# Kernel optimization log

Hardware: AMD Instinct MI355X
Metric: run time of the kernel (lower is better)

## Reference

```python
import jax, jax.numpy as jnp
import numpy as np

# physical constants (init_kwargs)
M1 = 1.0; M2 = 1.0; M3 = 1.0
L1 = 1.0; L2 = 1.0; L3 = 1.0
G = 9.81


def _kin(td):
    # td: [6] = (theta1, theta2, theta3, dth1, dth2, dth3)
    th, dth = td[:3], td[3:]
    dx1 = dth[0] * L1 * jnp.cos(th[0])
    dy1 = dth[0] * L1 * jnp.sin(th[0])
    dx2 = dx1 + dth[1] * L2 * jnp.cos(th[1])
    dy2 = dy1 + dth[1] * L2 * jnp.sin(th[1])
    dx3 = dx2 + dth[2] * L3 * jnp.cos(th[2])
    dy3 = dy2 + dth[2] * L3 * jnp.sin(th[2])
    vs1 = dx1 * dx1 + dy1 * dy1
    vs2 = dx2 * dx2 + dy2 * dy2
    vs3 = dx3 * dx3 + dy3 * dy3
    return 0.5 * (M1 * vs1 + M2 * vs2 + M3 * vs3)


def _pot(td):
    th = td[:3]
    y1 = -L1 * jnp.cos(th[0])
    y2 = y1 - L2 * jnp.cos(th[1])
    y3 = y2 - L3 * jnp.cos(th[2])
    return (M1 * G * (y1 + L1)
            + M2 * G * (y2 + L1 + L2)
            + M3 * G * (y3 + L1 + L2 + L3))


def _hamiltonian(y):
    # y: [6] = (theta, p_theta). Mass matrix = Hessian of kin w.r.t. velocity slots.
    Mmat = jax.hessian(_kin)(y)[3:6, 3:6]          # 3x3 mass matrix M(theta)
    p = y[3:6]
    dth = p @ jnp.linalg.inv(Mmat)                 # p_theta -> d_theta (M symmetric)
    K = _kin(jnp.concatenate([y[:3], dth]))
    return K + _pot(y)


def _dyn(y):
    g = jax.grad(_hamiltonian)(y)                  # dH/d(theta,p)
    return jnp.concatenate([g[3:6], -g[:3]])       # (dq, dp)


def setup_inputs() -> dict:
    key = jax.random.key(0)
    y = jax.random.normal(key, (2097152, 6), dtype=jnp.float32)
    t = jnp.zeros((1,), dtype=jnp.float32)
    return {"t": t, "y": y}


def reference(t, y):
    # t is unused by the dynamics (autonomous system), kept for API fidelity.
    return jax.vmap(_dyn)(y)
```

## Files before the change

kernel.cpp:

```cpp
#include <hip/hip_runtime.h>


#define GACC 9.81f

typedef float f32x4 __attribute__((ext_vector_type(4)));

__device__ __forceinline__ void dyn6(float th1, float th2, float th3,
                                     float p1, float p2, float p3,
                                     float* __restrict__ o) {
    float s1, c1, s2, c2, s3, c3;
    __sincosf(th1, &s1, &c1);
    __sincosf(th2, &s2, &c2);
    __sincosf(th3, &s3, &c3);
    float c12 = c1 * c2 + s1 * s2, s12 = s1 * c2 - c1 * s2;
    float c13 = c1 * c3 + s1 * s3, s13 = s1 * c3 - c1 * s3;
    float c23 = c2 * c3 + s2 * s3, s23 = s2 * c3 - c2 * s3;
    float A11 = 2.0f - c23 * c23;
    float A12 = c23 * c13 - 2.0f * c12;
    float A13 = 2.0f * (c12 * c23 - c13);
    float A22 = 3.0f - c13 * c13;
    float A23 = 2.0f * c12 * c13 - 3.0f * c23;
    float A33 = 6.0f - 4.0f * c12 * c12;
    float det = 3.0f * A11 + 2.0f * c12 * A12 + c13 * A13;
    float inv = 1.0f / det;
    float dth1 = (A11 * p1 + A12 * p2 + A13 * p3) * inv;
    float dth2 = (A12 * p1 + A22 * p2 + A23 * p3) * inv;
    float dth3 = (A13 * p1 + A23 * p2 + A33 * p3) * inv;
    o[0] = dth1;
    o[1] = dth2;
    o[2] = dth3;
    float t12 = dth1 * dth2 * s12;
    float t13 = dth1 * dth3 * s13;
    float t23 = dth2 * dth3 * s23;
    o[3] = -2.0f * t12 - t13 - 3.0f * GACC * s1;
    o[4] =  2.0f * t12 - t23 - 2.0f * GACC * s2;
    o[5] =  t13 + t23 - GACC * s3;
}

#define WFENCE() __builtin_amdgcn_fence(__ATOMIC_SEQ_CST, "wavefront")

__global__ __launch_bounds__(256, 6) void pend3_kernel(const f32x4* __restrict__ y4,
                                                       f32x4* __restrict__ out4,
                                                       int nTiles) {
    __shared__ f32x4 s[768];
    const int wave = threadIdx.x >> 6;
    const int lane = threadIdx.x & 63;
    f32x4* sw = s + wave * 192;

    for (int tile = blockIdx.x; tile < nTiles; tile += gridDim.x) {
        const size_t gbase = (size_t)tile * 768 + wave * 192;

#pragma unroll
        for (int k = 0; k < 3; ++k)
            sw[lane + 64 * k] = y4[gbase + lane + 64 * k];
        WFENCE();

        const int j0 = 3 * lane;
        f32x4 a = sw[j0];
        f32x4 b = sw[j0 + 1];
        f32x4 c = sw[j0 + 2];

        float o0[6], o1[6];
        dyn6(a.x, a.y, a.z, a.w, b.x, b.y, o0);
        dyn6(b.z, b.w, c.x, c.y, c.z, c.w, o1);

        f32x4 r0 = {o0[0], o0[1], o0[2], o0[3]};
        f32x4 r1 = {o0[4], o0[5], o1[0], o1[1]};
        f32x4 r2 = {o1[2], o1[3], o1[4], o1[5]};
        sw[j0]     = r0;
        sw[j0 + 1] = r1;
        sw[j0 + 2] = r2;
        WFENCE();

#pragma unroll
        for (int k = 0; k < 3; ++k) {
            f32x4 v = sw[lane + 64 * k];
            __builtin_nontemporal_store(v, &out4[gbase + lane + 64 * k]);
        }
        WFENCE();
    }
}

extern "C" void kernel_launch(void* const* d_in, const int* in_sizes, int n_in,
                              void* d_out, int out_size, void* d_ws, size_t ws_size,
                              hipStream_t stream) {
    const f32x4* y4 = (const f32x4*)d_in[1];
    f32x4* out4 = (f32x4*)d_out;
    int nQuads = in_sizes[1] / 4;
    int nTiles = nQuads / 768;
    int grid = nTiles < 2048 ? nTiles : 2048;
    pend3_kernel<<<grid, 256, 0, stream>>>(y4, out4, nTiles);
}
```

Baseline: 20.82 us.

## Process two tiles per block with all loads issued upfront, no grid-stride loop

Replaces the persistent grid-stride loop with a fixed grid where each block handles exactly two 768-quad tiles. Both tiles' global loads are issued up front into registers so the second tile's memory latency overlaps the first tile's compute and stores. It drops the occupancy hint from the launch bounds and assumes the input size is a multiple of 1536 quads, with no tail handling.

```diff
diff --git a/kernel.cpp b/kernel.cpp
--- a/kernel.cpp
+++ b/kernel.cpp
@@ -39,46 +39,61 @@
 
 #define WFENCE() __builtin_amdgcn_fence(__ATOMIC_SEQ_CST, "wavefront")
 
-__global__ __launch_bounds__(256, 6) void pend3_kernel(const f32x4* __restrict__ y4,
-                                                       f32x4* __restrict__ out4,
-                                                       int nTiles) {
+__device__ __forceinline__ void process_tile(f32x4* __restrict__ sw, int lane,
+                                             f32x4* __restrict__ outp) {
+    const int j0 = 3 * lane;
+    f32x4 a = sw[j0];
+    f32x4 b = sw[j0 + 1];
+    f32x4 c = sw[j0 + 2];
+
+    float o0[6], o1[6];
+    dyn6(a.x, a.y, a.z, a.w, b.x, b.y, o0);
+    dyn6(b.z, b.w, c.x, c.y, c.z, c.w, o1);
+
+    f32x4 r0 = {o0[0], o0[1], o0[2], o0[3]};
+    f32x4 r1 = {o0[4], o0[5], o1[0], o1[1]};
+    f32x4 r2 = {o1[2], o1[3], o1[4], o1[5]};
+    sw[j0]     = r0;
+    sw[j0 + 1] = r1;
+    sw[j0 + 2] = r2;
+    WFENCE();
+
+#pragma unroll
+    for (int k = 0; k < 3; ++k) {
+        f32x4 v = sw[lane + 64 * k];
+        __builtin_nontemporal_store(v, &outp[lane + 64 * k]);
+    }
+    WFENCE();
+}
+
+__global__ __launch_bounds__(256) void pend3_kernel(const f32x4* __restrict__ y4,
+                                                    f32x4* __restrict__ out4) {
     __shared__ f32x4 s[768];
-    const int wave = threadIdx.x >> 6;
-    const int lane = threadIdx.x & 63;
+    const int wave = (int)(threadIdx.x >> 6);
+    const int lane = (int)(threadIdx.x & 63);
     f32x4* sw = s + wave * 192;
 
-    for (int tile = blockIdx.x; tile < nTiles; tile += gridDim.x) {
-        const size_t gbase = (size_t)tile * 768 + wave * 192;
+    const size_t g0 = (size_t)blockIdx.x * 1536 + wave * 192;
+    const size_t g1 = g0 + 768;
 
-#pragma unroll
-        for (int k = 0; k < 3; ++k)
-            sw[lane + 64 * k] = y4[gbase + lane + 64 * k];
-        WFENCE();
+    f32x4 A0 = y4[g0 + lane];
+    f32x4 A1 = y4[g0 + lane + 64];
+    f32x4 A2 = y4[g0 + lane + 128];
+    f32x4 B0 = y4[g1 + lane];
+    f32x4 B1 = y4[g1 + lane + 64];
+    f32x4 B2 = y4[g1 + lane + 128];
 
-        const int j0 = 3 * lane;
-        f32x4 a = sw[j0];
-        f32x4 b = sw[j0 + 1];
-        f32x4 c = sw[j0 + 2];
+    sw[lane]       = A0;
+    sw[lane + 64]  = A1;
+    sw[lane + 128] = A2;
+    WFENCE();
+    process_tile(sw, lane, out4 + g0);
 
-        float o0[6], o1[6];
-        dyn6(a.x, a.y, a.z, a.w, b.x, b.y, o0);
-        dyn6(b.z, b.w, c.x, c.y, c.z, c.w, o1);
-
-        f32x4 r0 = {o0[0], o0[1], o0[2], o0[3]};
-        f32x4 r1 = {o0[4], o0[5], o1[0], o1[1]};
-        f32x4 r2 = {o1[2], o1[3], o1[4], o1[5]};
-        sw[j0]     = r0;
-        sw[j0 + 1] = r1;
-        sw[j0 + 2] = r2;
-        WFENCE();
-
-#pragma unroll
-        for (int k = 0; k < 3; ++k) {
-            f32x4 v = sw[lane + 64 * k];
-            __builtin_nontemporal_store(v, &out4[gbase + lane + 64 * k]);
-        }
-        WFENCE();
-    }
+    sw[lane]       = B0;
+    sw[lane + 64]  = B1;
+    sw[lane + 128] = B2;
+    WFENCE();
+    process_tile(sw, lane, out4 + g1);
 }
 
 extern "C" void kernel_launch(void* const* d_in, const int* in_sizes, int n_in,
@@ -87,7 +102,6 @@
     const f32x4* y4 = (const f32x4*)d_in[1];
     f32x4* out4 = (f32x4*)d_out;
     int nQuads = in_sizes[1] / 4;
-    int nTiles = nQuads / 768;
-    int grid = nTiles < 2048 ? nTiles : 2048;
-    pend3_kernel<<<grid, 256, 0, stream>>>(y4, out4, nTiles);
+    int grid = nQuads / 1536;
+    pend3_kernel<<<grid, 256, 0, stream>>>(y4, out4);
 }
```

After: 21.09 us. No clear change (+1.3%).
